# Kernel optimization log

Measured on AMD Instinct MI355X. Metric: run time of the kernel, lower is better.

## Reference

```python
import jax, jax.numpy as jnp
import numpy as np

NUM_LAYERS = 3
CHANNELS = 8
IN_CHANNELS = 8
MASK_OUT_STRIDE = 4
WEIGHT_NUMS = [(IN_CHANNELS + 2) * CHANNELS, CHANNELS * CHANNELS, CHANNELS]  # [80, 64, 8]
BIAS_NUMS = [CHANNELS, CHANNELS, 1]
NUM_GEN = sum(WEIGHT_NUMS) + sum(BIAS_NUMS)  # 169


def parse_params(params, weight_nums, bias_nums, channels):
    # params: [n_inst, sum(weight_nums)+sum(bias_nums)]
    n = params.shape[0]
    sizes = list(weight_nums) + list(bias_nums)
    splits = jnp.split(params, np.cumsum(sizes)[:-1].tolist(), axis=1)
    L = len(weight_nums)
    ws, bs = [], []
    for l in range(L):
        cout = channels if l < L - 1 else 1
        ws.append(splits[l].reshape(n, cout, -1))       # [n, cout, cin]
        bs.append(splits[L + l].reshape(n, cout))        # [n, cout]
    return ws, bs


def mask_head(x, ws, bs):
    # x: [n, cin, HW]; per-instance 1x1 convs == batched small GEMMs
    x_concat = None
    L = len(ws)
    for i, (w, b) in enumerate(zip(ws, bs)):
        x = jnp.einsum('noc,nch->noh', w, x) + b[:, :, None]
        if i < L - 1:
            x = jax.nn.relu(x)
        if i == L - 2:
            x_concat = x
    return x, x_concat


def aligned_bilinear(x, factor):
    # faithful port of AdelaiDet aligned_bilinear (align_corners=True interp)
    if factor == 1:
        return x
    n, c, h, w = x.shape
    x = jnp.pad(x, ((0, 0), (0, 0), (0, 1), (0, 1)), mode='edge')  # [h+1, w+1]
    oh, ow = factor * h + 1, factor * w + 1

    def interp_axis(arr, out_len, axis):
        # align_corners=True with out = factor*in - factor + 1 -> src = dst/factor exactly
        pos = jnp.arange(out_len) / factor
        i0 = jnp.floor(pos).astype(jnp.int32)
        i1 = jnp.minimum(i0 + 1, arr.shape[axis] - 1)
        frac = (pos - i0).astype(arr.dtype)
        a0 = jnp.take(arr, i0, axis=axis)
        a1 = jnp.take(arr, i1, axis=axis)
        shp = [1] * arr.ndim
        shp[axis] = out_len
        frac = frac.reshape(shp)
        return a0 * (1 - frac) + a1 * frac

    x = interp_axis(x, oh, 2)
    x = interp_axis(x, ow, 3)
    p = factor // 2
    x = jnp.pad(x, ((0, 0), (0, 0), (p, 0), (p, 0)), mode='edge')
    return x[:, :, :oh - 1, :ow - 1]


def setup_inputs() -> dict:
    key = jax.random.key(0)
    k1, k2, k3, k4, k5, k6 = jax.random.split(key, 6)
    N, Cin, H, W = 2, IN_CHANNELS, 100, 152
    n_inst = 128
    return {
        'mask_feats_body': jax.random.normal(k1, (N, Cin, H, W), dtype=jnp.float32),
        'mask_feats_edge': jax.random.normal(k2, (N, Cin, H, W), dtype=jnp.float32),
        'mask_head_params': jax.random.normal(k3, (n_inst, 2 * NUM_GEN + 81), dtype=jnp.float32) * 0.2,
        'inst_locations': jax.random.uniform(k4, (n_inst, 2), dtype=jnp.float32) * jnp.array([W * 8.0, H * 8.0]),
        'sizes_of_interest': jnp.array([64.0, 128.0, 256.0, 512.0, 1024.0], dtype=jnp.float32),
        'im_inds': jax.random.randint(k5, (n_inst,), 0, N, dtype=jnp.int32),
        'fpn_levels': jax.random.randint(k6, (n_inst,), 0, 5, dtype=jnp.int32),
        'mask_feat_stride': 8,
    }


def reference(mask_feats_body, mask_feats_edge, mask_head_params, inst_locations,
              sizes_of_interest, im_inds, fpn_levels, mask_feat_stride):
    N, Cin, H, W = mask_feats_body.shape
    n_inst = mask_head_params.shape[0]
    stride = mask_feat_stride

    # compute_locations: (x, y) grid at feature stride, offset stride//2
    shifts_x = jnp.arange(W, dtype=jnp.float32) * stride + stride // 2
    shifts_y = jnp.arange(H, dtype=jnp.float32) * stride + stride // 2
    sy, sx = jnp.meshgrid(shifts_y, shifts_x, indexing='ij')
    locations = jnp.stack([sx.reshape(-1), sy.reshape(-1)], axis=1)  # [HW, 2]

    rel = inst_locations[:, None, :] - locations[None, :, :]          # [n, HW, 2]
    rel = jnp.transpose(rel, (0, 2, 1))                               # [n, 2, HW]
    soi = sizes_of_interest[fpn_levels]                               # [n]
    rel = rel / soi[:, None, None]

    fb = mask_feats_body[im_inds].reshape(n_inst, Cin, H * W)
    fe = mask_feats_edge[im_inds].reshape(n_inst, Cin, H * W)
    inp_b = jnp.concatenate([rel, fb], axis=1)   # [n, Cin+2, HW]
    inp_e = jnp.concatenate([rel, fe], axis=1)

    wb, bb = parse_params(mask_head_params[:, :NUM_GEN], WEIGHT_NUMS, BIAS_NUMS, CHANNELS)
    we, be = parse_params(mask_head_params[:, NUM_GEN:2 * NUM_GEN], WEIGHT_NUMS, BIAS_NUMS, CHANNELS)
    wf, bf = parse_params(mask_head_params[:, 2 * NUM_GEN:], WEIGHT_NUMS[1:], BIAS_NUMS[1:], CHANNELS)

    logits_b, concat_b = mask_head(inp_b, wb, bb)
    logits_e, concat_e = mask_head(inp_e, we, be)
    logits_f, _ = mask_head(concat_b + concat_e, wf, bf)

    factor = mask_feat_stride // MASK_OUT_STRIDE
    outs = []
    for l in (logits_b, logits_e, logits_f):
        l = l.reshape(n_inst, 1, H, W)
        outs.append(jax.nn.sigmoid(aligned_bilinear(l, factor)))
    return tuple(outs)
```

## Files before the change

### kernel.cpp

```cpp
#include <hip/hip_runtime.h>
#include <hip/hip_bf16.h>
#include <hip/hip_fp16.h>

#define CIN      8
#define HH       100
#define WW       152
#define HWSZ     (HH * WW)
#define OHGT     200
#define OWID     304
#define PPI      419
#define OUT_PER_INST (OHGT * OWID)

#define RSTRIP   5
#define TROWS    6
#define NSTRIPS  20
#define QPT      38
#define P1THREADS (TROWS * QPT)
#define P2ITEMS  (3 * RSTRIP * 76)


typedef float vf4 __attribute__((ext_vector_type(4)));

__device__ __forceinline__ vf4 fma4(float w, vf4 x, vf4 a) { return w * x + a; }
__device__ __forceinline__ vf4 relu4(vf4 x) {
    vf4 r; r.x = fmaxf(x.x, 0.f); r.y = fmaxf(x.y, 0.f);
    r.z = fmaxf(x.z, 0.f); r.w = fmaxf(x.w, 0.f); return r;
}

__global__ __launch_bounds__(256) void dmh_fused4_kernel(
    const float* __restrict__ fbody,
    const float* __restrict__ fedge,
    const float* __restrict__ params,
    const float* __restrict__ locs,
    const float* __restrict__ soi_tab,
    const int*   __restrict__ im_inds,
    const int*   __restrict__ fpn_levels,
    float* __restrict__ out,
    int n_inst)
{
    const int s   = blockIdx.x;
    const int n   = blockIdx.y;
    const int tid = threadIdx.x;
    const int r0  = RSTRIP * s;

    __shared__ float slog[3][TROWS][WW];

    const float* __restrict__ p = params + (size_t)n * PPI;
    const int   im      = im_inds[n];
    const float inv_soi = 1.0f / soi_tab[fpn_levels[n]];
    const float sx = (locs[2 * n]     - 4.0f) * inv_soi;
    const float sy = (locs[2 * n + 1] - 4.0f) * inv_soi;
    const float k8 = 8.0f * inv_soi;

    if (tid < P1THREADS) {
        const int rl = tid / QPT;
        const int c  = (tid - rl * QPT) * 4;
        const int r  = min(r0 + rl, HH - 1);
        const int px = r * WW + c;

        const float dx0 = sx - (float)c * k8;
        const vf4 dx = { dx0, dx0 - k8, dx0 - 2.f * k8, dx0 - 3.f * k8 };
        const float dyv = sy - (float)r * k8;
        const vf4 dy = { dyv, dyv, dyv, dyv };

        const float* __restrict__ fb = fbody + (size_t)im * CIN * HWSZ + px;
        const float* __restrict__ fe = fedge + (size_t)im * CIN * HWSZ + px;

        vf4 inb[10], ine[8];
        inb[0] = dx; inb[1] = dy;
        #pragma unroll
        for (int k = 0; k < 8; ++k)
            inb[k + 2] = *(const vf4*)(fb + k * HWSZ);
        #pragma unroll
        for (int k = 0; k < 8; ++k)
            ine[k] = *(const vf4*)(fe + k * HWSZ);

        vf4 h1[8];

        #pragma unroll
        for (int o = 0; o < 8; ++o) {
            vf4 a = p[152 + o];
            #pragma unroll
            for (int k = 0; k < 10; ++k) a = fma4(p[o * 10 + k], inb[k], a);
            h1[o] = relu4(a);
        }
        vf4 h2b[8];
        #pragma unroll
        for (int o = 0; o < 8; ++o) {
            vf4 a = p[160 + o];
            #pragma unroll
            for (int k = 0; k < 8; ++k) a = fma4(p[80 + o * 8 + k], h1[k], a);
            h2b[o] = relu4(a);
        }
        vf4 lb = p[168];
        #pragma unroll
        for (int k = 0; k < 8; ++k) lb = fma4(p[144 + k], h2b[k], lb);

        #pragma unroll
        for (int o = 0; o < 8; ++o) {
            vf4 a = p[169 + 152 + o];
            a = fma4(p[169 + o * 10 + 0], dx, a);
            a = fma4(p[169 + o * 10 + 1], dy, a);
            #pragma unroll
            for (int k = 0; k < 8; ++k) a = fma4(p[169 + o * 10 + 2 + k], ine[k], a);
            h1[o] = relu4(a);
        }
        vf4 le = p[169 + 168];
        #pragma unroll
        for (int o = 0; o < 8; ++o) {
            vf4 a = p[169 + 160 + o];
            #pragma unroll
            for (int k = 0; k < 8; ++k) a = fma4(p[169 + 80 + o * 8 + k], h1[k], a);
            const vf4 he = relu4(a);
            le = fma4(p[169 + 144 + o], he, le);
            h2b[o] = h2b[o] + he;
        }

        vf4 hf[8];
        #pragma unroll
        for (int o = 0; o < 8; ++o) {
            vf4 a = p[410 + o];
            #pragma unroll
            for (int k = 0; k < 8; ++k) a = fma4(p[338 + o * 8 + k], h2b[k], a);
            hf[o] = relu4(a);
        }
        vf4 lf = p[418];
        #pragma unroll
        for (int k = 0; k < 8; ++k) lf = fma4(p[402 + k], hf[k], lf);

        *(vf4*)&slog[0][rl][c] = lb;
        *(vf4*)&slog[1][rl][c] = le;
        *(vf4*)&slog[2][rl][c] = lf;
    }
    __syncthreads();

    for (int it = tid; it < P2ITEMS; it += 256) {
        const int h   = it / (RSTRIP * 76);
        const int rem = it - h * (RSTRIP * 76);
        const int rr  = rem / 76;
        const int q   = rem - rr * 76;
        const int r   = r0 + rr;

        const int cm = max(2 * q - 1, 0);
        const int c0 = 2 * q;
        const int cp = min(2 * q + 1, WW - 1);

        const float Lm0 = slog[h][rr][cm],     L00 = slog[h][rr][c0],     Lp0 = slog[h][rr][cp];
        const float Lm1 = slog[h][rr + 1][cm], L01 = slog[h][rr + 1][c0], Lp1 = slog[h][rr + 1][cp];

        const float a0 = 0.5f * (Lm0 + L00);
        const float a1 = L00;
        const float a2 = 0.5f * (L00 + Lp0);
        const float a3 = Lp0;
        const float m  = 0.5f * (Lm0 + Lm1);
        const float z  = 0.5f * (L00 + L01);
        const float pz = 0.5f * (Lp0 + Lp1);
        const float b0 = 0.5f * (m + z);
        const float b1 = z;
        const float b2 = 0.5f * (z + pz);
        const float b3 = pz;

        vf4 A, B;
        A.x = 1.0f / (1.0f + __expf(-a0));
        A.y = 1.0f / (1.0f + __expf(-a1));
        A.z = 1.0f / (1.0f + __expf(-a2));
        A.w = 1.0f / (1.0f + __expf(-a3));
        B.x = 1.0f / (1.0f + __expf(-b0));
        B.y = 1.0f / (1.0f + __expf(-b1));
        B.z = 1.0f / (1.0f + __expf(-b2));
        B.w = 1.0f / (1.0f + __expf(-b3));

        float* __restrict__ O = out + ((size_t)h * n_inst + n) * OUT_PER_INST;
        const int xq = 4 * q;
        __builtin_nontemporal_store(A, (vf4*)(O + (size_t)(2 * r + 1) * OWID + xq));
        if (r == 0)
            __builtin_nontemporal_store(A, (vf4*)(O + xq));
        if (r < HH - 1)
            __builtin_nontemporal_store(B, (vf4*)(O + (size_t)(2 * r + 2) * OWID + xq));
    }
}

extern "C" void kernel_launch(void* const* d_in, const int* in_sizes, int n_in,
                              void* d_out, int out_size, void* d_ws, size_t ws_size,
                              hipStream_t stream) {
    const float* fbody   = (const float*)d_in[0];
    const float* fedge   = (const float*)d_in[1];
    const float* params  = (const float*)d_in[2];
    const float* locs    = (const float*)d_in[3];
    const float* soi     = (const float*)d_in[4];
    const int*   im_inds = (const int*)d_in[5];
    const int*   fpn     = (const int*)d_in[6];

    const int n_inst = in_sizes[5];

    dim3 grid(NSTRIPS, n_inst);
    dmh_fused4_kernel<<<grid, dim3(256), 0, stream>>>(
        fbody, fedge, params, locs, soi, im_inds, fpn,
        (float*)d_out, n_inst);
}
```

Before: 42.81 us.

## Compute per-instance mask-head MLPs with fp16 MFMA via packed block weight matrices

Replaces the per-thread scalar FMA evaluation of the body, edge and fused 1x1-conv stacks with four 16x16x32 fp16 MFMA instructions per 16-pixel chunk. The body and edge layers are packed into block-diagonal A matrices, with intermediates round-tripped through a small per-wave LDS scratch. The aim is to move the FMA-heavy phase onto matrix cores, at the cost of fp16 precision, scalar (non-vectorized) global feature loads, and extra LDS traffic and conversions. The upsample/sigmoid phase is unchanged.

```diff
diff --git a/kernel.cpp b/kernel.cpp
--- a/kernel.cpp
+++ b/kernel.cpp
@@ -14,20 +14,18 @@
 #define RSTRIP   5
 #define TROWS    6
 #define NSTRIPS  20
-#define QPT      38
-#define P1THREADS (TROWS * QPT)
+#define TILEPX   (TROWS * WW)
+#define NCHUNK   57
 #define P2ITEMS  (3 * RSTRIP * 76)
 
 
-typedef float vf4 __attribute__((ext_vector_type(4)));
-
-__device__ __forceinline__ vf4 fma4(float w, vf4 x, vf4 a) { return w * x + a; }
-__device__ __forceinline__ vf4 relu4(vf4 x) {
-    vf4 r; r.x = fmaxf(x.x, 0.f); r.y = fmaxf(x.y, 0.f);
-    r.z = fmaxf(x.z, 0.f); r.w = fmaxf(x.w, 0.f); return r;
-}
-
-__global__ __launch_bounds__(256) void dmh_fused4_kernel(
+typedef float    vf4   __attribute__((ext_vector_type(4)));
+typedef float    f32x4 __attribute__((ext_vector_type(4)));
+typedef _Float16 f16x8 __attribute__((ext_vector_type(8)));
+typedef _Float16 f16x4 __attribute__((ext_vector_type(4)));
+
+
+__global__ __launch_bounds__(256) void dmh_mfma_kernel(
     const float* __restrict__ fbody,
     const float* __restrict__ fedge,
     const float* __restrict__ params,
@@ -38,12 +36,22 @@
     float* __restrict__ out,
     int n_inst)
 {
-    const int s   = blockIdx.x;
-    const int n   = blockIdx.y;
-    const int tid = threadIdx.x;
-    const int r0  = RSTRIP * s;
-
-    __shared__ float slog[3][TROWS][WW];
+    const int s    = blockIdx.x;
+    const int n    = blockIdx.y;
+    const int tid  = threadIdx.x;
+    const int r0   = RSTRIP * s;
+    const int lane = tid & 63;
+    const int wid  = tid >> 6;
+    const int row  = lane & 15;
+    const int g    = lane >> 4;
+
+    __shared__ float    slogf[3 * TILEPX];
+    __shared__ _Float16 scratch[4 * 512];
+
+    _Float16* sc = scratch + wid * 512;
+
+    #pragma unroll
+    for (int z = 0; z < 8; ++z) sc[lane * 8 + z] = (_Float16)0.f;
 
     const float* __restrict__ p = params + (size_t)n * PPI;
     const int   im      = im_inds[n];
@@ -51,86 +59,86 @@
     const float sx = (locs[2 * n]     - 4.0f) * inv_soi;
     const float sy = (locs[2 * n + 1] - 4.0f) * inv_soi;
     const float k8 = 8.0f * inv_soi;
-
-    if (tid < P1THREADS) {
-        const int rl = tid / QPT;
-        const int c  = (tid - rl * QPT) * 4;
-        const int r  = min(r0 + rl, HH - 1);
-        const int px = r * WW + c;
-
-        const float dx0 = sx - (float)c * k8;
-        const vf4 dx = { dx0, dx0 - k8, dx0 - 2.f * k8, dx0 - 3.f * k8 };
-        const float dyv = sy - (float)r * k8;
-        const vf4 dy = { dyv, dyv, dyv, dyv };
-
-        const float* __restrict__ fb = fbody + (size_t)im * CIN * HWSZ + px;
-        const float* __restrict__ fe = fedge + (size_t)im * CIN * HWSZ + px;
-
-        vf4 inb[10], ine[8];
-        inb[0] = dx; inb[1] = dy;
+    const float* __restrict__ fb_base = fbody + (size_t)im * CIN * HWSZ;
+    const float* __restrict__ fe_base = fedge + (size_t)im * CIN * HWSZ;
+
+    f16x8 A1, A2, A3, A4;
+    #pragma unroll
+    for (int j = 0; j < 8; ++j) {
+        const int k = g * 8 + j;
+        float a1 = 0.f, a2 = 0.f, a3 = 0.f, a4 = 0.f;
+        if (row < 8) {
+            if (k < 10) a1 = p[row * 10 + k];
+            if (k < 8)  { a2 = p[80 + row * 8 + k]; a3 = p[338 + row * 8 + k]; }
+        } else {
+            if (k >= 10 && k < 20) a1 = p[169 + (row - 8) * 10 + (k - 10)];
+            if (k >= 8  && k < 16) a2 = p[169 + 80 + (row - 8) * 8 + (k - 8)];
+        }
+        if (row == 0 && k < 8)             a4 = p[144 + k];
+        if (row == 1 && k >= 8  && k < 16) a4 = p[169 + 144 + (k - 8)];
+        if (row == 2 && k >= 16 && k < 24) a4 = p[402 + (k - 16)];
+        A1[j] = (_Float16)a1; A2[j] = (_Float16)a2;
+        A3[j] = (_Float16)a3; A4[j] = (_Float16)a4;
+    }
+    f32x4 C1, C2, C3, C4;
+    #pragma unroll
+    for (int rI = 0; rI < 4; ++rI) {
+        const int R = g * 4 + rI;
+        C1[rI] = (R < 8) ? p[152 + R] : p[169 + 152 + (R - 8)];
+        C2[rI] = (R < 8) ? p[160 + R] : p[169 + 160 + (R - 8)];
+        C3[rI] = (R < 8) ? p[410 + R] : 0.f;
+        C4[rI] = (R == 0) ? p[168] : (R == 1) ? p[169 + 168] : (R == 2) ? p[418] : 0.f;
+    }
+
+    for (int ck = wid; ck < NCHUNK; ck += 4) {
+        const int pxl = ck * 16 + row;
+        const int rl  = pxl / WW;
+        const int cc  = pxl - rl * WW;
+        const int rr  = min(r0 + rl, HH - 1);
+        const int gpx = rr * WW + cc;
+        const float dxv = sx - (float)cc * k8;
+        const float dyv = sy - (float)rr * k8;
+
         #pragma unroll
-        for (int k = 0; k < 8; ++k)
-            inb[k + 2] = *(const vf4*)(fb + k * HWSZ);
-        #pragma unroll
-        for (int k = 0; k < 8; ++k)
-            ine[k] = *(const vf4*)(fe + k * HWSZ);
-
-        vf4 h1[8];
-
-        #pragma unroll
-        for (int o = 0; o < 8; ++o) {
-            vf4 a = p[152 + o];
-            #pragma unroll
-            for (int k = 0; k < 10; ++k) a = fma4(p[o * 10 + k], inb[k], a);
-            h1[o] = relu4(a);
+        for (int t = 0; t < 4; ++t) {
+            const int chn = g + 4 * t;
+            const float v = (chn < 8) ? fb_base[chn * HWSZ + gpx]
+                                      : fe_base[(chn - 8) * HWSZ + gpx];
+            const int k = (chn < 8) ? (2 + chn) : (4 + chn);
+            sc[row * 32 + k] = (_Float16)v;
         }
-        vf4 h2b[8];
-        #pragma unroll
-        for (int o = 0; o < 8; ++o) {
-            vf4 a = p[160 + o];
-            #pragma unroll
-            for (int k = 0; k < 8; ++k) a = fma4(p[80 + o * 8 + k], h1[k], a);
-            h2b[o] = relu4(a);
+        if (g == 0) { sc[row * 32 + 0]  = (_Float16)dxv; sc[row * 32 + 1]  = (_Float16)dyv; }
+        if (g == 1) { sc[row * 32 + 10] = (_Float16)dxv; sc[row * 32 + 11] = (_Float16)dyv; }
+
+        f16x8 B = *(const f16x8*)(sc + row * 32 + g * 8);
+        f32x4 d = __builtin_amdgcn_mfma_f32_16x16x32_f16(A1, B, C1, 0, 0, 0);
+        f16x4 t4;
+        t4[0] = (_Float16)fmaxf(d.x, 0.f); t4[1] = (_Float16)fmaxf(d.y, 0.f);
+        t4[2] = (_Float16)fmaxf(d.z, 0.f); t4[3] = (_Float16)fmaxf(d.w, 0.f);
+        *(f16x4*)(sc + row * 32 + g * 4) = t4;
+
+        B = *(const f16x8*)(sc + row * 32 + g * 8);
+        d = __builtin_amdgcn_mfma_f32_16x16x32_f16(A2, B, C2, 0, 0, 0);
+        t4[0] = (_Float16)fmaxf(d.x, 0.f); t4[1] = (_Float16)fmaxf(d.y, 0.f);
+        t4[2] = (_Float16)fmaxf(d.z, 0.f); t4[3] = (_Float16)fmaxf(d.w, 0.f);
+        *(f16x4*)(sc + row * 32 + g * 4) = t4;
+
+        const f16x8 rA = *(const f16x8*)(sc + row * 32 + g * 8);
+        const int  rbo = (g < 3) ? (row * 32 + g * 8 + 8) : (row * 32 + 24);
+        const f16x8 rB = *(const f16x8*)(sc + rbo);
+        B = rA + rB;
+        d = __builtin_amdgcn_mfma_f32_16x16x32_f16(A3, B, C3, 0, 0, 0);
+        t4[0] = (_Float16)fmaxf(d.x, 0.f); t4[1] = (_Float16)fmaxf(d.y, 0.f);
+        t4[2] = (_Float16)fmaxf(d.z, 0.f); t4[3] = (_Float16)fmaxf(d.w, 0.f);
+        *(f16x4*)(sc + 16 + row * 32 + g * 4) = t4;
+
+        B = *(const f16x8*)(sc + row * 32 + g * 8);
+        d = __builtin_amdgcn_mfma_f32_16x16x32_f16(A4, B, C4, 0, 0, 0);
+        if (g == 0) {
+            slogf[pxl]              = d.x;
+            slogf[TILEPX + pxl]     = d.y;
+            slogf[2 * TILEPX + pxl] = d.z;
         }
-        vf4 lb = p[168];
-        #pragma unroll
-        for (int k = 0; k < 8; ++k) lb = fma4(p[144 + k], h2b[k], lb);
-
-        #pragma unroll
-        for (int o = 0; o < 8; ++o) {
-            vf4 a = p[169 + 152 + o];
-            a = fma4(p[169 + o * 10 + 0], dx, a);
-            a = fma4(p[169 + o * 10 + 1], dy, a);
-            #pragma unroll
-            for (int k = 0; k < 8; ++k) a = fma4(p[169 + o * 10 + 2 + k], ine[k], a);
-            h1[o] = relu4(a);
-        }
-        vf4 le = p[169 + 168];
-        #pragma unroll
-        for (int o = 0; o < 8; ++o) {
-            vf4 a = p[169 + 160 + o];
-            #pragma unroll
-            for (int k = 0; k < 8; ++k) a = fma4(p[169 + 80 + o * 8 + k], h1[k], a);
-            const vf4 he = relu4(a);
-            le = fma4(p[169 + 144 + o], he, le);
-            h2b[o] = h2b[o] + he;
-        }
-
-        vf4 hf[8];
-        #pragma unroll
-        for (int o = 0; o < 8; ++o) {
-            vf4 a = p[410 + o];
-            #pragma unroll
-            for (int k = 0; k < 8; ++k) a = fma4(p[338 + o * 8 + k], h2b[k], a);
-            hf[o] = relu4(a);
-        }
-        vf4 lf = p[418];
-        #pragma unroll
-        for (int k = 0; k < 8; ++k) lf = fma4(p[402 + k], hf[k], lf);
-
-        *(vf4*)&slog[0][rl][c] = lb;
-        *(vf4*)&slog[1][rl][c] = le;
-        *(vf4*)&slog[2][rl][c] = lf;
     }
     __syncthreads();
 
@@ -144,9 +152,11 @@
         const int cm = max(2 * q - 1, 0);
         const int c0 = 2 * q;
         const int cp = min(2 * q + 1, WW - 1);
-
-        const float Lm0 = slog[h][rr][cm],     L00 = slog[h][rr][c0],     Lp0 = slog[h][rr][cp];
-        const float Lm1 = slog[h][rr + 1][cm], L01 = slog[h][rr + 1][c0], Lp1 = slog[h][rr + 1][cp];
+        const float* L0 = slogf + h * TILEPX + rr * WW;
+        const float* L1 = L0 + WW;
+
+        const float Lm0 = L0[cm], L00 = L0[c0], Lp0 = L0[cp];
+        const float Lm1 = L1[cm], L01 = L1[c0], Lp1 = L1[cp];
 
         const float a0 = 0.5f * (Lm0 + L00);
         const float a1 = L00;
@@ -160,15 +170,15 @@
         const float b2 = 0.5f * (z + pz);
         const float b3 = pz;
 
-        vf4 A, B;
-        A.x = 1.0f / (1.0f + __expf(-a0));
-        A.y = 1.0f / (1.0f + __expf(-a1));
-        A.z = 1.0f / (1.0f + __expf(-a2));
-        A.w = 1.0f / (1.0f + __expf(-a3));
-        B.x = 1.0f / (1.0f + __expf(-b0));
-        B.y = 1.0f / (1.0f + __expf(-b1));
-        B.z = 1.0f / (1.0f + __expf(-b2));
-        B.w = 1.0f / (1.0f + __expf(-b3));
+        vf4 A, Bv;
+        A.x  = 1.0f / (1.0f + __expf(-a0));
+        A.y  = 1.0f / (1.0f + __expf(-a1));
+        A.z  = 1.0f / (1.0f + __expf(-a2));
+        A.w  = 1.0f / (1.0f + __expf(-a3));
+        Bv.x = 1.0f / (1.0f + __expf(-b0));
+        Bv.y = 1.0f / (1.0f + __expf(-b1));
+        Bv.z = 1.0f / (1.0f + __expf(-b2));
+        Bv.w = 1.0f / (1.0f + __expf(-b3));
 
         float* __restrict__ O = out + ((size_t)h * n_inst + n) * OUT_PER_INST;
         const int xq = 4 * q;
@@ -176,7 +186,7 @@
         if (r == 0)
             __builtin_nontemporal_store(A, (vf4*)(O + xq));
         if (r < HH - 1)
-            __builtin_nontemporal_store(B, (vf4*)(O + (size_t)(2 * r + 2) * OWID + xq));
+            __builtin_nontemporal_store(Bv, (vf4*)(O + (size_t)(2 * r + 2) * OWID + xq));
     }
 }
 
@@ -194,7 +204,7 @@
     const int n_inst = in_sizes[5];
 
     dim3 grid(NSTRIPS, n_inst);
-    dmh_fused4_kernel<<<grid, dim3(256), 0, stream>>>(
+    dmh_mfma_kernel<<<grid, dim3(256), 0, stream>>>(
         fbody, fedge, params, locs, soi, im_inds, fpn,
         (float*)d_out, n_inst);
 }
```

Measured after the change: 75.34 us. 76.0% more time.
